# Optimization experiments

Hardware: AMD Instinct MI355X
Metric: run time of the kernel (lower is better)

The kernel has to match this reference:

```python
import jax, jax.numpy as jnp
import numpy as np
import math

MUL = 16                      # num_in_features == num_out_features
LDIMS = (1, 3, 5)             # 0e, 1o, 2e  (lmax = 2)
FEAT = MUL * sum(LDIMS)       # 144 = irreps dim = number_of_basis
PATHS = [(0,0,0),(1,1,0),(2,2,0),
         (0,1,1),(1,0,1),(1,2,1),(2,1,1),
         (0,2,2),(1,1,2),(2,0,2),(2,2,2)]
DOT_PATHS = [(0,0,0),(1,1,0),(2,2,0)]

# ---------- real Wigner-3j / Clebsch-Gordan (e3nn convention), numpy precompute ----------

def _su2_cg(j1, m1, j2, m2, j3, m3):
    if m3 != m1 + m2:
        return 0.0
    f = math.factorial
    vmin = max(-j1 + j2 + m3, -j1 + m1, 0)
    vmax = min(j2 + j3 + m1, j3 - j1 + j2, j3 + m3)
    C = math.sqrt((2*j3+1) * f(j3+j1-j2) * f(j3-j1+j2) * f(j1+j2-j3)
                  * f(j3+m3) * f(j3-m3)
                  / (f(j1+j2+j3+1) * f(j1-m1) * f(j1+m1) * f(j2-m2) * f(j2+m2)))
    S = 0.0
    for v in range(vmin, vmax + 1):
        S += (-1.0)**(v + j2 + m2) * f(j2+j3+m1-v) * f(j1-m1+v) / (
            f(v) * f(j3-j1+j2-v) * f(j3+m3-v) * f(v+j1-j2-m3))
    return C * S

def _qmat(l):
    # complex -> real spherical-harmonic change of basis (e3nn convention)
    q = np.zeros((2*l+1, 2*l+1), dtype=np.complex128)
    for m in range(-l, 0):
        q[l+m, l+abs(m)] = 1.0/math.sqrt(2)
        q[l+m, l-abs(m)] = -1j/math.sqrt(2)
    q[l, l] = 1.0
    for m in range(1, l+1):
        q[l+m, l+abs(m)] = (-1)**m/math.sqrt(2)
        q[l+m, l-abs(m)] = 1j*(-1)**m/math.sqrt(2)
    return (-1j)**l * q

def _real_w3j(l1, l2, l3):
    C = np.zeros((2*l1+1, 2*l2+1, 2*l3+1))
    for i, m1 in enumerate(range(-l1, l1+1)):
        for j, m2 in enumerate(range(-l2, l2+1)):
            for k, m3 in enumerate(range(-l3, l3+1)):
                C[i, j, k] = _su2_cg(l1, m1, l2, m2, l3, m3)
    Cr = np.einsum('ij,kl,mn,ikn->jlm', _qmat(l1), _qmat(l2),
                   np.conj(_qmat(l3).T), C.astype(np.complex128))
    Cr = np.real(Cr)
    return (Cr / np.linalg.norm(Cr)).astype(np.float32)  # unit Frobenius norm (3j convention)

W3J = {p: _real_w3j(*p) for p in set(PATHS)}

# ---------- fully connected tensor product (component/element normalization) ----------

def _split(x):
    # blocked layout: [mul x 0e | mul x 1o | mul x 2e]
    n = x.shape[0]
    xs, o = [], 0
    for d in LDIMS:
        xs.append(x[:, o:o + MUL*d].reshape(n, MUL, d))
        o += MUL * d
    return xs

def _fctp(x1, x2, W):
    # W: [11, u, v, w] stacked per PATHS
    xs1, xs2 = _split(x1), _split(x2)
    n = x1.shape[0]
    n_paths = {l3: sum(1 for p in PATHS if p[2] == l3) for l3 in range(3)}
    outs = [None, None, None]
    for i, (l1, l2, l3) in enumerate(PATHS):
        C = jnp.asarray(W3J[(l1, l2, l3)])          # [i, j, k]
        scale = math.sqrt((2*l3 + 1) / (n_paths[l3] * MUL * MUL))
        a = jnp.einsum('nvj,ijk->nivk', xs2[l2], C)      # [n, i, v, k]
        b = jnp.einsum('nui,nivk->nuvk', xs1[l1], a)     # [n, u, v, k]
        o = scale * jnp.einsum('nuvk,uvw->nwk', b, W[i]) # [n, w, k]
        outs[l3] = o if outs[l3] is None else outs[l3] + o
    return jnp.concatenate([o.reshape(n, -1) for o in outs], axis=1)  # [n, 9*MUL]

def _dot(x1, x2, Wd):
    # FCTP(irreps_input, irreps_input, '0e'): paths (0,0,0),(1,1,0),(2,2,0), out mul = 1
    xs1, xs2 = _split(x1), _split(x2)
    fan = 3 * MUL * MUL
    acc = 0.0
    for i, (l1, l2, l3) in enumerate(DOT_PATHS):
        C = jnp.asarray(W3J[(l1, l2, l3)])[:, :, 0]      # [i, j]
        t = jnp.einsum('nui,ij,nvj->nuv', xs1[l1], C, xs2[l2])
        acc = acc + jnp.einsum('nuv,uv->n', t, Wd[i])
    return (acc * math.sqrt(1.0 / fan))[:, None]         # [n, 1]

def setup_inputs() -> dict:
    key = jax.random.key(0)
    ks = jax.random.split(key, 8)
    N = 50000
    return {
        'nodes_features': jax.random.normal(ks[0], (N, FEAT), jnp.float32),
        'degree_matrix': jax.random.normal(ks[1], (N,), jnp.float32),
        'edges_features_distance': jax.random.normal(ks[2], (N,), jnp.float32),
        'edges_features_bond': jax.random.normal(ks[3], (N,), jnp.float32),
        'w_q': jax.random.normal(ks[4], (11, MUL, MUL, MUL), jnp.float32),
        'w_k': jax.random.normal(ks[5], (11, MUL, MUL, MUL), jnp.float32),
        'w_v': jax.random.normal(ks[6], (11, MUL, MUL, MUL), jnp.float32),
        'w_dot': jax.random.normal(ks[7], (3, MUL, MUL), jnp.float32),
    }

def reference(nodes_features, degree_matrix, edges_features_distance,
              edges_features_bond, w_q, w_k, w_v, w_dot):
    # degree_matrix / edges_features_* are unused by the original forward
    x = nodes_features
    q = _fctp(x, x, w_q)                   # tp_q(x, x)
    k = _fctp(x, x, w_k)                   # tp_k(x, x)
    v = _fctp(x, x, w_v)                   # tp(x, x)
    d = _dot(q, k, w_dot)                  # [n, 1]
    e = jnp.exp(d / math.sqrt(float(FEAT)))
    attn = e / (e + 1e-10)                 # sum over last dim of size 1 + eps
    out = attn * v                         # dropout is identity in eval mode
    out = out.reshape(-1, MUL)             # view(-1, num_heads * num_out_features)
    return jax.nn.elu(out)                 # [9n, MUL]
```

## Files before the change

### kernel.cpp

```cpp
#include <hip/hip_runtime.h>
#include <math.h>

#define NP 11
#define NN 8

__device__ __constant__ int g_l1[NP]   = {0,1,2,0,1,1,2,0,1,2,2};
__device__ __constant__ int g_l2[NP]   = {0,1,2,1,0,2,1,2,1,0,2};
__device__ __constant__ int g_l3[NP]   = {0,0,0,1,1,1,1,2,2,2,2};
__device__ __constant__ int g_coff[NP] = {0,1,10,35,44,53,98,143,168,213,238};

typedef _Float16 half8 __attribute__((ext_vector_type(8)));
typedef _Float16 h2 __attribute__((ext_vector_type(2)));
typedef float f32x4 __attribute__((ext_vector_type(4)));

__device__ double dfact(int n){ double r=1.0; for(int i=2;i<=n;++i) r*=(double)i; return r; }

__device__ double su2_cg(int j1,int m1,int j2,int m2,int j3,int m3){
  if(m1+m2!=m3) return 0.0;
  int vmin=-j1+j2+m3; if(-j1+m1>vmin) vmin=-j1+m1; if(vmin<0) vmin=0;
  int vmax=j2+j3+m1; int t=j3-j1+j2; if(t<vmax) vmax=t; t=j3+m3; if(t<vmax) vmax=t;
  double C = sqrt((double)(2*j3+1)*dfact(j3+j1-j2)*dfact(j3-j1+j2)*dfact(j1+j2-j3)
      *dfact(j3+m3)*dfact(j3-m3)
      /(dfact(j1+j2+j3+1)*dfact(j1-m1)*dfact(j1+m1)*dfact(j2-m2)*dfact(j2+m2)));
  double S=0.0;
  for(int v=vmin;v<=vmax;++v){
    double sg = ((v+j2+m2)&1)? -1.0:1.0;
    S += sg*dfact(j2+j3+m1-v)*dfact(j1-m1+v)
        /(dfact(v)*dfact(j3-j1+j2-v)*dfact(j3+m3-v)*dfact(v+j1-j2-m3));
  }
  return C*S;
}

__device__ void qelem(int l,int r,int c,double &re,double &im){
  int m=r-l; double a=0.0,b=0.0; const double s=0.70710678118654752440;
  if(m<0){ if(c==l-m) a=s; else if(c==l+m) b=-s; }
  else if(m==0){ if(c==l) a=1.0; }
  else { double sg=(m&1)?-1.0:1.0; if(c==l+m) a=sg*s; else if(c==l-m) b=sg*s; }
  if(l==1){ double tt=a; a=b; b=-tt; }
  else if(l==2){ a=-a; b=-b; }
  re=a; im=b;
}

__global__ void w3j_init(float* __restrict__ ws){
  int p=blockIdx.x;
  int l1=g_l1[p], l2=g_l2[p], l3=g_l3[p];
  int d1=2*l1+1, d2=2*l2+1, d3=2*l3+1;
  int tot=d1*d2*d3;
  __shared__ double cg[125];
  __shared__ double outv[125];
  __shared__ double nrm;
  for(int t=threadIdx.x;t<tot;t+=blockDim.x){
    int i=t/(d2*d3), k=(t/d3)%d2, n=t%d3;
    cg[t]=su2_cg(l1,i-l1,l2,k-l2,l3,n-l3);
  }
  __syncthreads();
  for(int t=threadIdx.x;t<tot;t+=blockDim.x){
    int a=t/(d2*d3), b=(t/d3)%d2, c=t%d3;
    double sre=0.0;
    for(int i=0;i<d1;++i){ double q1r,q1i; qelem(l1,i,a,q1r,q1i);
      for(int k=0;k<d2;++k){ double q2r,q2i; qelem(l2,k,b,q2r,q2i);
        double pr=q1r*q2r-q1i*q2i, pi=q1r*q2i+q1i*q2r;
        for(int n=0;n<d3;++n){ double q3r,q3i; qelem(l3,n,c,q3r,q3i);
          sre += (pr*q3r + pi*q3i) * cg[(i*d2+k)*d3+n];
        }
      }
    }
    outv[t]=sre;
  }
  __syncthreads();
  if(threadIdx.x==0){
    double s=0.0; for(int t=0;t<tot;++t) s+=outv[t]*outv[t];
    nrm=sqrt(s);
  }
  __syncthreads();
  for(int t=threadIdx.x;t<tot;t+=blockDim.x)
    ws[g_coff[p]+t]=(float)(outv[t]/nrm);
}

__global__ void dtype_probe5(const unsigned short* p0,const unsigned short* p1,
                             const unsigned short* p2,const unsigned short* p3,
                             const unsigned short* p4,
                             int n0,int n1,int n2,int n3,int n4,
                             float* __restrict__ flags){
  __shared__ int cnt;
  const unsigned short* ps[5]={p0,p1,p2,p3,p4};
  int ns[5]={n0,n1,n2,n3,n4};
  int b=blockIdx.x;
  const unsigned short* p=ps[b]; int nelem=ns[b];
  if(threadIdx.x==0) cnt=0;
  __syncthreads();
  int M = nelem < 4096 ? nelem : 4096;
  int c=0;
  for(int t=threadIdx.x;t<M;t+=blockDim.x){
    unsigned e=((unsigned)p[t]>>7)&0xFFu;
    if(e!=0u && (e<0x70u || e>0x8Eu)) ++c;
  }
  atomicAdd(&cnt,c);
  __syncthreads();
  if(threadIdx.x==0) flags[b] = (cnt*8 > M) ? 1.0f : 0.0f;
}

__device__ __forceinline__ float bfu(unsigned int v){ return __uint_as_float(v<<16); }
__device__ __forceinline__ unsigned int rne16(float f){
  unsigned int ui=__float_as_uint(f);
  return (ui+0x7fffu+((ui>>16)&1u))>>16;
}
__device__ __forceinline__ unsigned short h16(float f){
  _Float16 h=(_Float16)f;
  return __builtin_bit_cast(unsigned short,h);
}

__global__ void c_pack(const float* __restrict__ c3j, unsigned int* __restrict__ cgh){
  int p=blockIdx.x;
  int d1=2*g_l1[p]+1, d2=2*g_l2[p]+1, d3=2*g_l3[p]+1;
  const float scl_[3]={0.03608439182435161f,0.05412658773652741f,0.06987712429686843f};
  float s=scl_[g_l3[p]];
  int tot=d1*d2*d3;
  for(int t=threadIdx.x;t<tot;t+=64){
    unsigned int h=(unsigned int)h16(c3j[g_coff[p]+t]*s);
    cgh[g_coff[p]+t]=h|(h<<16);
  }
}

__global__ void w_prep(const unsigned short* __restrict__ wq,
                       const unsigned short* __restrict__ wk,
                       const unsigned short* __restrict__ wv,
                       const float* __restrict__ flags,
                       unsigned int* __restrict__ wpre){
  int p=blockIdx.x, tp=blockIdx.y;
  const unsigned short* ww=(tp==0)?wq:((tp==1)?wk:wv);
  int f32=flags[tp]!=0.0f;
  unsigned int* dst=wpre+(size_t)(p*3+tp)*2240;
  for(int t=threadIdx.x;t<2048;t+=256){
    int w=t>>7, c=t&127, u=c&15, vp=c>>4;
    int i0=(u*16+2*vp)*16+w, i1=i0+16;
    float f0,f1;
    if(f32){
      const float* wf=(const float*)ww+(size_t)p*4096;
      f0=wf[i0]; f1=wf[i1];
    }else{
      const unsigned short* wsp=ww+(size_t)p*4096;
      f0=bfu(wsp[i0]); f1=bfu(wsp[i1]);
    }
    dst[w*140+c]=(unsigned int)h16(f0)|((unsigned int)h16(f1)<<16);
  }
}

template<int D1,int D2,int D3>
__device__ __forceinline__ void fusedAB(const unsigned int* __restrict__ sXp,
                                        const unsigned int* __restrict__ sXd,
                                        const unsigned int* __restrict__ cgp,
                                        unsigned int* __restrict__ sAu,
                                        int wave, int lane, int nvalid){
  constexpr int O1=(D1==1)?0:((D1==3)?16:64);
  constexpr int O2P=(D2==1)?0:((D2==3)?8:32);
  const int nn=lane>>3, vp=lane&7;
  if(nn>=nvalid) return;
  h2 x2p[D2];
  #pragma unroll
  for(int j=0;j<D2;++j) x2p[j]=__builtin_bit_cast(h2,sXp[nn*76+O2P+vp*D2+j]);
  const int u0=wave*2;
  h2 x1a[D1],x1b[D1];
  #pragma unroll
  for(int i=0;i<D1;++i){
    x1a[i]=__builtin_bit_cast(h2,sXd[nn*148+O1+u0*D1+i]);
    x1b[i]=__builtin_bit_cast(h2,sXd[nn*148+O1+(u0+1)*D1+i]);
  }
  h2 acc0[D3],acc1[D3];
  #pragma unroll
  for(int k=0;k<D3;++k){ acc0[k]=(h2){(_Float16)0.f,(_Float16)0.f}; acc1[k]=acc0[k]; }
  #pragma unroll
  for(int i=0;i<D1;++i){
    #pragma unroll
    for(int k=0;k<D3;++k){
      h2 ar=(h2){(_Float16)0.f,(_Float16)0.f};
      #pragma unroll
      for(int j=0;j<D2;++j)
        ar+=__builtin_bit_cast(h2,cgp[(i*D2+j)*D3+k])*x2p[j];
      acc0[k]+=x1a[i]*ar;
      acc1[k]+=x1b[i]*ar;
    }
  }
  #pragma unroll
  for(int k=0;k<D3;++k){
    uint2 st;
    st.x=__builtin_bit_cast(unsigned int,acc0[k]);
    st.y=__builtin_bit_cast(unsigned int,acc1[k]);
    *(uint2*)(sAu+(k*8+nn)*140+vp*16+u0)=st;
  }
}

template<int L3>
__device__ __forceinline__ void stage2_acc(const unsigned int* __restrict__ sAu,
                                           const unsigned int* __restrict__ wp_path,
                                           f32x4& a0, f32x4& a1,
                                           int n16, int quad, int wave){
  constexpr int P=(L3+1)*3;
  if(wave<P){
    int tp=wave%3, Mt=wave/3;
    const unsigned int* ap=sAu+(Mt*16+n16)*140+quad*4;
    const uint4* bp=(const uint4*)(wp_path+tp*2240+n16*140+quad*4);
    uint4 b[8];
    #pragma unroll
    for(int ks=0;ks<8;++ks) b[ks]=bp[ks*4];
    f32x4 a=a0;
    #pragma unroll
    for(int ks=0;ks<8;++ks)
      a=__builtin_amdgcn_mfma_f32_16x16x32_f16(
          *reinterpret_cast<const half8*>(ap+ks*16),
          __builtin_bit_cast(half8,b[ks]),a,0,0,0);
    a0=a;
  }
  if(L3==2 && wave==0){
    const unsigned int* ap=sAu+(2*16+n16)*140+quad*4;
    const uint4* bp=(const uint4*)(wp_path+2*2240+n16*140+quad*4);
    uint4 b[8];
    #pragma unroll
    for(int ks=0;ks<8;++ks) b[ks]=bp[ks*4];
    f32x4 a=a1;
    #pragma unroll
    for(int ks=0;ks<8;++ks)
      a=__builtin_amdgcn_mfma_f32_16x16x32_f16(
          *reinterpret_cast<const half8*>(ap+ks*16),
          __builtin_bit_cast(half8,b[ks]),a,0,0,0);
    a1=a;
  }
}

template<int L3>
__device__ __forceinline__ void stage2_out(const f32x4& a0, const f32x4& a1,
                                           float* __restrict__ sO,
                                           int n16, int quad, int wave){
  constexpr int D3=2*L3+1;
  constexpr int OO=(L3==0)?0:((L3==1)?16:64);
  constexpr int P=(L3+1)*3;
  if(wave<P){
    int tp=wave%3, Mt=wave/3;
    #pragma unroll
    for(int reg=0;reg<4;++reg){
      int row=Mt*16+quad*4+reg;
      int k=row>>3, node=row&7;
      if(k<D3) sO[node*440+tp*144+OO+n16*D3+k]=a0[reg];
    }
  }
  if(L3==2 && wave==0){
    #pragma unroll
    for(int reg=0;reg<4;++reg){
      int row=32+quad*4+reg;
      int k=row>>3, node=row&7;
      if(k<D3) sO[node*440+2*144+OO+n16*D3+k]=a1[reg];
    }
  }
}

__global__ __launch_bounds__(512,6) void tfn_main(
    const unsigned short* __restrict__ xin,
    const unsigned int* __restrict__ wpre,
    const unsigned int* __restrict__ cgh,
    const unsigned short* __restrict__ wd,
    const float* __restrict__ c3j,
    unsigned short* __restrict__ outp, int N)
{
  __shared__ __align__(16) unsigned int sAu[48*140];
  __shared__ float sO[NN*440];
  __shared__ __align__(8) unsigned int sXp[NN*76];
  __shared__ __align__(8) unsigned int sXd[NN*148];
  __shared__ float sWd[768];

  const int tid=threadIdx.x;
  const int wave=tid>>6, lane=tid&63;
  const int n16=lane&15, quad=lane>>4;
  const int node0=blockIdx.x*NN;
  const int nvalid=(N-node0)<NN?(N-node0):NN;

  const int xf32 = c3j[363]!=0.0f;
  const int df32 = c3j[367]!=0.0f;

  float* scratch=sO;
  if(!xf32){
    for(int t=tid;t<NN*36;t+=512){
      int nn=t/36, w4=t%36;
      if(nn<nvalid){
        uint2 u=((const uint2*)(xin+(size_t)(node0+nn)*144))[w4];
        float* dst=&scratch[nn*144+w4*4];
        dst[0]=bfu(u.x&0xffffu); dst[1]=bfu(u.x>>16);
        dst[2]=bfu(u.y&0xffffu); dst[3]=bfu(u.y>>16);
      }
    }
  }else{
    const float* xf=(const float*)xin;
    for(int t=tid;t<NN*144;t+=512){
      int nn=t/144, f=t%144;
      if(nn<nvalid) scratch[nn*144+f]=xf[(size_t)(node0+nn)*144+f];
    }
  }
  if(!df32){ for(int t=tid;t<768;t+=512) sWd[t]=bfu((unsigned int)wd[t]); }
  else     { const float* wdf=(const float*)wd; for(int t=tid;t<768;t+=512) sWd[t]=wdf[t]; }
  __syncthreads();

  for(int t=tid;t<NN*144;t+=512){
    int nn=t/144, f=t-nn*144;
    unsigned int h=(unsigned int)h16(scratch[t]);
    sXd[nn*148+f]=h|(h<<16);
  }
  for(int t=tid;t<NN*72;t+=512){
    int nn=t/72, g=t-nn*72;
    int fa,fb;
    if(g<8){ fa=2*g; fb=fa+1; }
    else if(g<32){ int gg=g-8; int vp=gg/3, j=gg-3*vp; fa=16+(2*vp)*3+j; fb=fa+3; }
    else { int gg=g-32; int vp=gg/5, j=gg-5*vp; fa=64+(2*vp)*5+j; fb=fa+5; }
    sXp[nn*76+g]=(unsigned int)h16(scratch[nn*144+fa])|((unsigned int)h16(scratch[nn*144+fb])<<16);
  }
  __syncthreads();

  #define PATH_STEP(P_,D1_,D2_,D3_) { \
    fusedAB<D1_,D2_,D3_>(sXp,sXd,cgh+g_coff[P_],sAu,wave,lane,nvalid); \
    __syncthreads(); \
    stage2_acc<(D3_-1)/2>(sAu,wpre+(size_t)P_*6720,a0,a1,n16,quad,wave); \
    __syncthreads(); }

  {
    f32x4 a0={0.f,0.f,0.f,0.f}, a1={0.f,0.f,0.f,0.f};
    PATH_STEP(0,1,1,1)
    PATH_STEP(1,3,3,1)
    PATH_STEP(2,5,5,1)
    stage2_out<0>(a0,a1,sO,n16,quad,wave);
  }
  {
    f32x4 a0={0.f,0.f,0.f,0.f}, a1={0.f,0.f,0.f,0.f};
    PATH_STEP(3,1,3,3)
    PATH_STEP(4,3,1,3)
    PATH_STEP(5,3,5,3)
    PATH_STEP(6,5,3,3)
    stage2_out<1>(a0,a1,sO,n16,quad,wave);
  }
  {
    f32x4 a0={0.f,0.f,0.f,0.f}, a1={0.f,0.f,0.f,0.f};
    PATH_STEP(7,1,5,5)
    PATH_STEP(8,3,3,5)
    PATH_STEP(9,5,1,5)
    PATH_STEP(10,5,5,5)
    stage2_out<2>(a0,a1,sO,n16,quad,wave);
  }
  #undef PATH_STEP
  __syncthreads();

  {
    int node=wave;
    if(node<nvalid){
      const float c0=c3j[0], c1=c3j[1], c2=c3j[10];
      const float* qv=sO+node*440;
      const float* kv=qv+144;
      const int v=lane&15, ug=lane>>4;
      float k0=kv[v];
      float k1[3],k2[5];
      #pragma unroll
      for(int j=0;j<3;++j) k1[j]=kv[16+v*3+j];
      #pragma unroll
      for(int m=0;m<5;++m) k2[m]=kv[64+v*5+m];
      float part=0.f;
      #pragma unroll
      for(int t=0;t<4;++t){
        int u=ug+4*t;
        float d0=qv[u]*k0;
        float d1=0.f;
        #pragma unroll
        for(int j=0;j<3;++j) d1+=qv[16+u*3+j]*k1[j];
        float d2=0.f;
        #pragma unroll
        for(int m=0;m<5;++m) d2+=qv[64+u*5+m]*k2[m];
        part+=sWd[u*16+v]*(c0*d0)+sWd[256+u*16+v]*(c1*d1)+sWd[512+u*16+v]*(c2*d2);
      }
      #pragma unroll
      for(int off=1;off<64;off<<=1) part+=__shfl_xor(part,off,64);
      float dd=part*0.03608439182435161f;
      float ex=dd*(1.0f/12.0f);
      ex=fminf(fmaxf(ex,-80.f),80.f);
      float e=expf(ex);
      float attn=e/(e+1e-10f);
      const float* vv=sO+node*440+288;
      if(!xf32){
        unsigned short* ob=outp+(size_t)(node0+node)*144;
        for(int f=lane;f<144;f+=64){
          float val=attn*vv[f];
          float r=(val>0.f)?val:expm1f(val);
          ob[f]=(unsigned short)rne16(r);
        }
      }else{
        float* ob=(float*)outp+(size_t)(node0+node)*144;
        for(int f=lane;f<144;f+=64){
          float val=attn*vv[f];
          ob[f]=(val>0.f)?val:expm1f(val);
        }
      }
    }
  }
}

extern "C" void kernel_launch(void* const* d_in, const int* in_sizes, int n_in,
                              void* d_out, int out_size, void* d_ws, size_t ws_size,
                              hipStream_t stream){
  (void)n_in; (void)out_size; (void)ws_size;
  const unsigned short* x =(const unsigned short*)d_in[0];
  const unsigned short* wq=(const unsigned short*)d_in[4];
  const unsigned short* wk=(const unsigned short*)d_in[5];
  const unsigned short* wv=(const unsigned short*)d_in[6];
  const unsigned short* wd=(const unsigned short*)d_in[7];
  float* c3j=(float*)d_ws;
  unsigned int* cgh=(unsigned int*)d_ws+1024;
  unsigned int* wpre=(unsigned int*)d_ws+2048;
  int N=in_sizes[0]/144;
  w3j_init<<<dim3(NP),dim3(128),0,stream>>>(c3j);
  dtype_probe5<<<dim3(5),dim3(256),0,stream>>>(x,wq,wk,wv,wd,
      in_sizes[0],in_sizes[4],in_sizes[5],in_sizes[6],in_sizes[7],c3j+363);
  c_pack<<<dim3(NP),dim3(64),0,stream>>>(c3j,cgh);
  w_prep<<<dim3(NP,3),dim3(256),0,stream>>>(wq,wk,wv,c3j+364,wpre);
  int nb=(N+NN-1)/NN;
  tfn_main<<<dim3(nb),dim3(512),0,stream>>>(x,wpre,cgh,wd,c3j,(unsigned short*)d_out,N);
}
```

Measured before the change: 385.2 us.

## Merge setup kernels, prefetch stage-2 weights early, and reorder intermediate smem layout

Combines the four setup kernels (Wigner-3j init, dtype probe, CG packing, weight prep) into one prep kernel. Each block probes its own weight dtype, and one block also probes x and w_dot. In the main kernel, each wave now loads its MFMA B-operand weight fragments from global memory before the fused stage-A compute and barrier, so that load latency overlaps with the A-stage work. The intermediate sAu tile moves from an interleaved uint2 layout to a u*8+vp column order, with the weight packing index changed to match. The aim is cheaper shared-memory stores, at the cost of holding more registers live across the barrier.

```diff
diff --git a/kernel.cpp b/kernel.cpp
--- a/kernel.cpp
+++ b/kernel.cpp
@@ -12,6 +12,16 @@
 typedef _Float16 half8 __attribute__((ext_vector_type(8)));
 typedef _Float16 h2 __attribute__((ext_vector_type(2)));
 typedef float f32x4 __attribute__((ext_vector_type(4)));
+
+__device__ __forceinline__ float bfu(unsigned int v){ return __uint_as_float(v<<16); }
+__device__ __forceinline__ unsigned int rne16(float f){
+  unsigned int ui=__float_as_uint(f);
+  return (ui+0x7fffu+((ui>>16)&1u))>>16;
+}
+__device__ __forceinline__ unsigned short h16(float f){
+  _Float16 h=(_Float16)f;
+  return __builtin_bit_cast(unsigned short,h);
+}
 
 __device__ double dfact(int n){ double r=1.0; for(int i=2;i<=n;++i) r*=(double)i; return r; }
 
@@ -41,53 +51,8 @@
   re=a; im=b;
 }
 
-__global__ void w3j_init(float* __restrict__ ws){
-  int p=blockIdx.x;
-  int l1=g_l1[p], l2=g_l2[p], l3=g_l3[p];
-  int d1=2*l1+1, d2=2*l2+1, d3=2*l3+1;
-  int tot=d1*d2*d3;
-  __shared__ double cg[125];
-  __shared__ double outv[125];
-  __shared__ double nrm;
-  for(int t=threadIdx.x;t<tot;t+=blockDim.x){
-    int i=t/(d2*d3), k=(t/d3)%d2, n=t%d3;
-    cg[t]=su2_cg(l1,i-l1,l2,k-l2,l3,n-l3);
-  }
-  __syncthreads();
-  for(int t=threadIdx.x;t<tot;t+=blockDim.x){
-    int a=t/(d2*d3), b=(t/d3)%d2, c=t%d3;
-    double sre=0.0;
-    for(int i=0;i<d1;++i){ double q1r,q1i; qelem(l1,i,a,q1r,q1i);
-      for(int k=0;k<d2;++k){ double q2r,q2i; qelem(l2,k,b,q2r,q2i);
-        double pr=q1r*q2r-q1i*q2i, pi=q1r*q2i+q1i*q2r;
-        for(int n=0;n<d3;++n){ double q3r,q3i; qelem(l3,n,c,q3r,q3i);
-          sre += (pr*q3r + pi*q3i) * cg[(i*d2+k)*d3+n];
-        }
-      }
-    }
-    outv[t]=sre;
-  }
-  __syncthreads();
-  if(threadIdx.x==0){
-    double s=0.0; for(int t=0;t<tot;++t) s+=outv[t]*outv[t];
-    nrm=sqrt(s);
-  }
-  __syncthreads();
-  for(int t=threadIdx.x;t<tot;t+=blockDim.x)
-    ws[g_coff[p]+t]=(float)(outv[t]/nrm);
-}
-
-__global__ void dtype_probe5(const unsigned short* p0,const unsigned short* p1,
-                             const unsigned short* p2,const unsigned short* p3,
-                             const unsigned short* p4,
-                             int n0,int n1,int n2,int n3,int n4,
-                             float* __restrict__ flags){
-  __shared__ int cnt;
-  const unsigned short* ps[5]={p0,p1,p2,p3,p4};
-  int ns[5]={n0,n1,n2,n3,n4};
-  int b=blockIdx.x;
-  const unsigned short* p=ps[b]; int nelem=ns[b];
-  if(threadIdx.x==0) cnt=0;
+__device__ int probe_f32(const unsigned short* __restrict__ p, int nelem, int* scnt){
+  if(threadIdx.x==0) *scnt=0;
   __syncthreads();
   int M = nelem < 4096 ? nelem : 4096;
   int c=0;
@@ -95,54 +60,88 @@
     unsigned e=((unsigned)p[t]>>7)&0xFFu;
     if(e!=0u && (e<0x70u || e>0x8Eu)) ++c;
   }
-  atomicAdd(&cnt,c);
+  atomicAdd(scnt,c);
   __syncthreads();
-  if(threadIdx.x==0) flags[b] = (cnt*8 > M) ? 1.0f : 0.0f;
-}
-
-__device__ __forceinline__ float bfu(unsigned int v){ return __uint_as_float(v<<16); }
-__device__ __forceinline__ unsigned int rne16(float f){
-  unsigned int ui=__float_as_uint(f);
-  return (ui+0x7fffu+((ui>>16)&1u))>>16;
-}
-__device__ __forceinline__ unsigned short h16(float f){
-  _Float16 h=(_Float16)f;
-  return __builtin_bit_cast(unsigned short,h);
-}
-
-__global__ void c_pack(const float* __restrict__ c3j, unsigned int* __restrict__ cgh){
-  int p=blockIdx.x;
-  int d1=2*g_l1[p]+1, d2=2*g_l2[p]+1, d3=2*g_l3[p]+1;
-  const float scl_[3]={0.03608439182435161f,0.05412658773652741f,0.06987712429686843f};
-  float s=scl_[g_l3[p]];
-  int tot=d1*d2*d3;
-  for(int t=threadIdx.x;t<tot;t+=64){
-    unsigned int h=(unsigned int)h16(c3j[g_coff[p]+t]*s);
-    cgh[g_coff[p]+t]=h|(h<<16);
-  }
-}
-
-__global__ void w_prep(const unsigned short* __restrict__ wq,
-                       const unsigned short* __restrict__ wk,
-                       const unsigned short* __restrict__ wv,
-                       const float* __restrict__ flags,
-                       unsigned int* __restrict__ wpre){
-  int p=blockIdx.x, tp=blockIdx.y;
+  return (*scnt*8 > M) ? 1 : 0;
+}
+
+__global__ void prep(const unsigned short* __restrict__ x,
+                     const unsigned short* __restrict__ wq,
+                     const unsigned short* __restrict__ wk,
+                     const unsigned short* __restrict__ wv,
+                     const unsigned short* __restrict__ wd,
+                     int nx,int nw,int nd,
+                     float* __restrict__ c3j, unsigned int* __restrict__ cgh,
+                     unsigned int* __restrict__ wpre){
+  const int p=blockIdx.x, tp=blockIdx.y;
+  __shared__ double cg[125];
+  __shared__ double outv[125];
+  __shared__ double nrm;
+  __shared__ int scnt;
+
   const unsigned short* ww=(tp==0)?wq:((tp==1)?wk:wv);
-  int f32=flags[tp]!=0.0f;
-  unsigned int* dst=wpre+(size_t)(p*3+tp)*2240;
-  for(int t=threadIdx.x;t<2048;t+=256){
-    int w=t>>7, c=t&127, u=c&15, vp=c>>4;
-    int i0=(u*16+2*vp)*16+w, i1=i0+16;
-    float f0,f1;
-    if(f32){
-      const float* wf=(const float*)ww+(size_t)p*4096;
-      f0=wf[i0]; f1=wf[i1];
-    }else{
-      const unsigned short* wsp=ww+(size_t)p*4096;
-      f0=bfu(wsp[i0]); f1=bfu(wsp[i1]);
-    }
-    dst[w*140+c]=(unsigned int)h16(f0)|((unsigned int)h16(f1)<<16);
+  const int f32 = probe_f32(ww,nw,&scnt);
+
+  {
+    unsigned int* dst=wpre+(size_t)(p*3+tp)*2240;
+    for(int t=threadIdx.x;t<2048;t+=256){
+      int w=t>>7, c=t&127;
+      int i0=c*32+w, i1=i0+16;
+      float f0,f1;
+      if(f32){
+        const float* wf=(const float*)ww+(size_t)p*4096;
+        f0=wf[i0]; f1=wf[i1];
+      }else{
+        const unsigned short* wsp=ww+(size_t)p*4096;
+        f0=bfu(wsp[i0]); f1=bfu(wsp[i1]);
+      }
+      dst[w*140+c]=(unsigned int)h16(f0)|((unsigned int)h16(f1)<<16);
+    }
+  }
+
+  if(tp==0){
+    int l1=g_l1[p], l2=g_l2[p], l3=g_l3[p];
+    int d1=2*l1+1, d2=2*l2+1, d3=2*l3+1;
+    int tot=d1*d2*d3;
+    for(int t=threadIdx.x;t<tot;t+=256){
+      int i=t/(d2*d3), k=(t/d3)%d2, n=t%d3;
+      cg[t]=su2_cg(l1,i-l1,l2,k-l2,l3,n-l3);
+    }
+    __syncthreads();
+    for(int t=threadIdx.x;t<tot;t+=256){
+      int a=t/(d2*d3), b=(t/d3)%d2, c=t%d3;
+      double sre=0.0;
+      for(int i=0;i<d1;++i){ double q1r,q1i; qelem(l1,i,a,q1r,q1i);
+        for(int k=0;k<d2;++k){ double q2r,q2i; qelem(l2,k,b,q2r,q2i);
+          double pr=q1r*q2r-q1i*q2i, pi=q1r*q2i+q1i*q2r;
+          for(int n=0;n<d3;++n){ double q3r,q3i; qelem(l3,n,c,q3r,q3i);
+            sre += (pr*q3r + pi*q3i) * cg[(i*d2+k)*d3+n];
+          }
+        }
+      }
+      outv[t]=sre;
+    }
+    __syncthreads();
+    if(threadIdx.x==0){
+      double s=0.0; for(int t=0;t<tot;++t) s+=outv[t]*outv[t];
+      nrm=sqrt(s);
+    }
+    __syncthreads();
+    const float scl_[3]={0.03608439182435161f,0.05412658773652741f,0.06987712429686843f};
+    float s=scl_[l3];
+    for(int t=threadIdx.x;t<tot;t+=256){
+      float val=(float)(outv[t]/nrm);
+      c3j[g_coff[p]+t]=val;
+      unsigned int h=(unsigned int)h16(val*s);
+      cgh[g_coff[p]+t]=h|(h<<16);
+    }
+  }
+
+  if(p==0 && tp==0){
+    int xf=probe_f32(x,nx,&scnt);
+    if(threadIdx.x==0) c3j[363]=(float)xf;
+    int df=probe_f32(wd,nd,&scnt);
+    if(threadIdx.x==0) c3j[367]=(float)df;
   }
 }
 
@@ -183,46 +182,41 @@
   }
   #pragma unroll
   for(int k=0;k<D3;++k){
-    uint2 st;
-    st.x=__builtin_bit_cast(unsigned int,acc0[k]);
-    st.y=__builtin_bit_cast(unsigned int,acc1[k]);
-    *(uint2*)(sAu+(k*8+nn)*140+vp*16+u0)=st;
+    sAu[(k*8+nn)*140+u0*8+vp]   =__builtin_bit_cast(unsigned int,acc0[k]);
+    sAu[(k*8+nn)*140+u0*8+vp+8] =__builtin_bit_cast(unsigned int,acc1[k]);
   }
 }
 
 template<int L3>
 __device__ __forceinline__ void stage2_acc(const unsigned int* __restrict__ sAu,
                                            const unsigned int* __restrict__ wp_path,
+                                           const uint4* __restrict__ bf,
                                            f32x4& a0, f32x4& a1,
                                            int n16, int quad, int wave){
   constexpr int P=(L3+1)*3;
   if(wave<P){
-    int tp=wave%3, Mt=wave/3;
+    int Mt=wave/3;
     const unsigned int* ap=sAu+(Mt*16+n16)*140+quad*4;
-    const uint4* bp=(const uint4*)(wp_path+tp*2240+n16*140+quad*4);
-    uint4 b[8];
-    #pragma unroll
-    for(int ks=0;ks<8;++ks) b[ks]=bp[ks*4];
     f32x4 a=a0;
     #pragma unroll
     for(int ks=0;ks<8;++ks)
       a=__builtin_amdgcn_mfma_f32_16x16x32_f16(
           *reinterpret_cast<const half8*>(ap+ks*16),
-          __builtin_bit_cast(half8,b[ks]),a,0,0,0);
+          __builtin_bit_cast(half8,bf[ks]),a,0,0,0);
     a0=a;
   }
   if(L3==2 && wave==0){
     const unsigned int* ap=sAu+(2*16+n16)*140+quad*4;
     const uint4* bp=(const uint4*)(wp_path+2*2240+n16*140+quad*4);
-    uint4 b[8];
-    #pragma unroll
-    for(int ks=0;ks<8;++ks) b[ks]=bp[ks*4];
+    uint4 b2[8];
+    #pragma unroll
+    for(int ks=0;ks<8;++ks) b2[ks]=bp[ks*4];
     f32x4 a=a1;
     #pragma unroll
     for(int ks=0;ks<8;++ks)
       a=__builtin_amdgcn_mfma_f32_16x16x32_f16(
           *reinterpret_cast<const half8*>(ap+ks*16),
-          __builtin_bit_cast(half8,b[ks]),a,0,0,0);
+          __builtin_bit_cast(half8,b2[ks]),a,0,0,0);
     a1=a;
   }
 }
@@ -314,9 +308,16 @@
   __syncthreads();
 
   #define PATH_STEP(P_,D1_,D2_,D3_) { \
+    const int PT=((D3_-1)/2+1)*3; \
+    uint4 bf[8]; \
+    if(wave<PT){ \
+      const uint4* bp=(const uint4*)(wpre+(size_t)P_*6720+(wave%3)*2240+n16*140+quad*4); \
+      bf[0]=bp[0];  bf[1]=bp[4];  bf[2]=bp[8];  bf[3]=bp[12]; \
+      bf[4]=bp[16]; bf[5]=bp[20]; bf[6]=bp[24]; bf[7]=bp[28]; \
+    } \
     fusedAB<D1_,D2_,D3_>(sXp,sXd,cgh+g_coff[P_],sAu,wave,lane,nvalid); \
     __syncthreads(); \
-    stage2_acc<(D3_-1)/2>(sAu,wpre+(size_t)P_*6720,a0,a1,n16,quad,wave); \
+    stage2_acc<(D3_-1)/2>(sAu,wpre+(size_t)P_*6720,bf,a0,a1,n16,quad,wave); \
     __syncthreads(); }
 
   {
@@ -410,11 +411,8 @@
   unsigned int* cgh=(unsigned int*)d_ws+1024;
   unsigned int* wpre=(unsigned int*)d_ws+2048;
   int N=in_sizes[0]/144;
-  w3j_init<<<dim3(NP),dim3(128),0,stream>>>(c3j);
-  dtype_probe5<<<dim3(5),dim3(256),0,stream>>>(x,wq,wk,wv,wd,
-      in_sizes[0],in_sizes[4],in_sizes[5],in_sizes[6],in_sizes[7],c3j+363);
-  c_pack<<<dim3(NP),dim3(64),0,stream>>>(c3j,cgh);
-  w_prep<<<dim3(NP,3),dim3(256),0,stream>>>(wq,wk,wv,c3j+364,wpre);
+  prep<<<dim3(NP,3),dim3(256),0,stream>>>(x,wq,wk,wv,wd,
+      in_sizes[0],in_sizes[4],in_sizes[7],c3j,cgh,wpre);
   int nb=(N+NN-1)/NN;
   tfn_main<<<dim3(nb),dim3(512),0,stream>>>(x,wpre,cgh,wd,c3j,(unsigned short*)d_out,N);
 }
```

After: 354.9 us, median of 2. 7.9% less time.
